# Optimization experiments

Hardware: AMD Instinct MI355X
Metric: run time of the kernel (lower is better)

## Reference

```python
import jax, jax.numpy as jnp
import numpy as np

B, N, C, H, NB = 8, 16384, 128, 512, 2  # batch, points, d_feat, mlp hidden, n_block
WIN, NH = 64, 4


def _bn(x, g, b, eps=1e-5):
    # BatchNorm1d in training mode: normalize per channel over (B, N)
    m = x.mean(axis=(0, 1))
    v = x.var(axis=(0, 1))
    return (x - m) * jax.lax.rsqrt(v + eps) * g + b


def _perm_batch(key, b, n):
    return jax.vmap(lambda k: jax.random.permutation(k, n))(jax.random.split(key, b)).astype(jnp.int32)


def setup_inputs():
    key = jax.random.key(0)
    ks = jax.random.split(key, 12)
    s = 0.02
    x = jax.random.normal(ks[0], (B, N, C), jnp.float32)
    z = jax.random.normal(ks[1], (B, N, 3), jnp.float32)
    idx_pa_1 = _perm_batch(ks[2], B, N)  # random permutation per batch row
    idx_pa_2 = _perm_batch(ks[3], B, N)
    qkv_w = jax.random.normal(ks[4], (NB, C, 3 * C), jnp.float32) * s
    proj_w = jax.random.normal(ks[5], (NB, C, C), jnp.float32) * s
    fc1_w = jax.random.normal(ks[6], (NB, C, H), jnp.float32) * s
    fc2_w = jax.random.normal(ks[7], (NB, H, C), jnp.float32) * s
    n1_g = jnp.ones((NB, C), jnp.float32)
    n1_b = jnp.zeros((NB, C), jnp.float32)
    n2_g = jnp.ones((NB, C), jnp.float32)
    n2_b = jnp.zeros((NB, C), jnp.float32)
    return {"x": x, "z": z, "idx_pa_1": idx_pa_1, "idx_pa_2": idx_pa_2,
            "qkv_w": qkv_w, "proj_w": proj_w, "fc1_w": fc1_w, "fc2_w": fc2_w,
            "n1_g": n1_g, "n1_b": n1_b, "n2_g": n2_g, "n2_b": n2_b}


def reference(x, z, idx_pa_1, idx_pa_2, qkv_w, proj_w, fc1_w, fc2_w, n1_g, n1_b, n2_g, n2_b):
    b, n, c = x.shape
    nh, dh, w = NH, c // NH, WIN
    nw = n // w
    scale = np.float32(1.0 / np.sqrt(dh))
    idx_re_1 = jnp.argsort(idx_pa_1, axis=1)  # inverse permutation
    idx_re_2 = jnp.argsort(idx_pa_2, axis=1)
    for i in range(NB):
        ip = idx_pa_1 if i % 2 == 0 else idx_pa_2
        ir = idx_re_1 if i % 2 == 0 else idx_re_2
        # SpaceExpansion: gather by random permutation
        x = jnp.take_along_axis(x, ip[:, :, None], axis=1)
        zz = jnp.take_along_axis(z, ip[:, :, None], axis=1)
        # windowed attention (pre-norm, residual)
        h = _bn(x, n1_g[i], n1_b[i])
        qkv = jnp.einsum('bnc,cd->bnd', h, qkv_w[i]).reshape(b, nw, w, 3, nh, dh)
        q, k, v = qkv[:, :, :, 0], qkv[:, :, :, 1], qkv[:, :, :, 2]
        att = jax.nn.softmax(jnp.einsum('bwqhd,bwkhd->bwhqk', q, k) * scale, axis=-1)
        o = jnp.einsum('bwhqk,bwkhd->bwqhd', att, v).reshape(b, n, c)
        x = x + jnp.einsum('bnc,cd->bnd', o, proj_w[i])
        # MLP (pre-norm, residual)
        h2 = _bn(x, n2_g[i], n2_b[i])
        x = x + jnp.einsum('bnh,hc->bnc', jax.nn.relu(jnp.einsum('bnc,ch->bnh', h2, fc1_w[i])), fc2_w[i])
        # SpaceReverse: scatter back via inverse permutation
        x = jnp.take_along_axis(x, ir[:, :, None], axis=1)
        z = jnp.take_along_axis(zz, ir[:, :, None], axis=1)
    return x, z
```

## Files before the change

### kernel.cpp

```cpp
#include <hip/hip_runtime.h>
#include <cstdint>
#include <cstddef>

typedef uint16_t u16;
typedef __bf16 bf16x8 __attribute__((ext_vector_type(8)));
typedef float f32x4 __attribute__((ext_vector_type(4)));
typedef unsigned short us4 __attribute__((ext_vector_type(4)));

#define NTOK 131072
#define CDIM 128
#define MFMA __builtin_amdgcn_mfma_f32_16x16x32_bf16

__device__ __forceinline__ u16 f2b(float f) {
    unsigned int x = __builtin_bit_cast(unsigned int, f);
    unsigned int r = (x + 0x7fffu + ((x >> 16) & 1u)) >> 16;
    return (u16)r;
}

__device__ __forceinline__ us4 pack_bn4(float4 v, const float* sc, const float* sh, int c) {
    us4 o;
    o.x = f2b(v.x * sc[c] + sh[c]);
    o.y = f2b(v.y * sc[c + 1] + sh[c + 1]);
    o.z = f2b(v.z * sc[c + 2] + sh[c + 2]);
    o.w = f2b(v.w * sc[c + 3] + sh[c + 3]);
    return o;
}

__global__ __launch_bounds__(256) void bn_init(const float* __restrict__ x,
                                               float* __restrict__ acc) {
    int tid = threadIdx.x;
    int c4 = tid & 31;
    int ro = tid >> 5;
    float4 s = {0.f, 0.f, 0.f, 0.f}, s2 = {0.f, 0.f, 0.f, 0.f};
    size_t base = ((size_t)blockIdx.x * 128 + ro) * 128 + c4 * 4;
#pragma unroll
    for (int it = 0; it < 16; ++it) {
        float4 v = *(const float4*)(x + base + (size_t)it * 1024);
        s.x += v.x; s.y += v.y; s.z += v.z; s.w += v.w;
        s2.x += v.x * v.x; s2.y += v.y * v.y; s2.z += v.z * v.z; s2.w += v.w * v.w;
    }
    __shared__ float4 a1[256], a2[256];
    a1[tid] = s; a2[tid] = s2;
    __syncthreads();
    if (tid < 128) {
        int col4 = tid >> 2, comp = tid & 3;
        float t1 = 0.f, t2 = 0.f;
#pragma unroll
        for (int r = 0; r < 8; ++r) {
            t1 += a1[r * 32 + col4][comp];
            t2 += a2[r * 32 + col4][comp];
        }
        float* st = acc + (blockIdx.x & 3) * 256;
        atomicAdd(st + tid, t1);
        atomicAdd(st + 128 + tid, t2);
    }
}

__global__ void bn_finalize(const float* __restrict__ acc, const float* __restrict__ g,
                            const float* __restrict__ b, float* __restrict__ scsh) {
    int c = threadIdx.x;
    const float invn = 1.0f / (float)NTOK;
    float s = acc[c] + acc[256 + c] + acc[512 + c] + acc[768 + c];
    float q = acc[128 + c] + acc[384 + c] + acc[640 + c] + acc[896 + c];
    float mean = s * invn;
    float var = q * invn - mean * mean;
    float sc = g[c] * rsqrtf(var + 1e-5f);
    scsh[c] = sc;
    scsh[128 + c] = b[c] - mean * sc;
}

__global__ __launch_bounds__(256) void wtrans(const float* __restrict__ w, u16* __restrict__ wt,
                                              int K, int N) {
    int t = blockIdx.x * 256 + threadIdx.x;
    if (t >= K * N) return;
    int n = t % N, k = t / N;
    wt[(size_t)n * K + k] = f2b(w[t]);
}

__global__ __launch_bounds__(256, 2) void attn_fused(
    const float* __restrict__ xsrc, float* __restrict__ xdst,
    const int* __restrict__ ip, const float* __restrict__ scsh,
    const u16* __restrict__ wq, const u16* __restrict__ wp,
    float* __restrict__ stat)
{
    __shared__ u16 hsh[64 * 128];
    __shared__ u16 qkp[4][5120];
    __shared__ u16 vt[4][32 * 72];
    __shared__ float sc[128], sh[128];
    __shared__ int ipl[64];

    int tid = threadIdx.x;
    int lane = tid & 63, wv = tid >> 6;
    int l15 = lane & 15, hi = lane >> 4;
    int b = blockIdx.x >> 8;

    if (tid < 128) { sc[tid] = scsh[tid]; sh[tid] = scsh[128 + tid]; }
    if (tid < 64) ipl[tid] = ip[blockIdx.x * 64 + tid];
    __syncthreads();

    int c4 = tid & 31;
#pragma unroll
    for (int p = 0; p < 8; ++p) {
        int row = p * 8 + (tid >> 5);
        int grow = (b << 14) + ipl[row];
        float4 v = *(const float4*)(xsrc + (size_t)grow * 128 + c4 * 4);
        us4 o = pack_bn4(v, sc, sh, c4 * 4);
        int byte = (c4 * 8) ^ ((row & 7) << 4);
        *(us4*)((char*)hsh + row * 256 + byte) = o;
    }
    __syncthreads();

    int nrow[6];
#pragma unroll
    for (int nt = 0; nt < 6; ++nt) nrow[nt] = (nt >> 1) * 128 + wv * 32 + (nt & 1) * 16;
    f32x4 acc[4][6];
#pragma unroll
    for (int q = 0; q < 4; ++q)
#pragma unroll
        for (int nt = 0; nt < 6; ++nt) acc[q][nt] = (f32x4){0.f, 0.f, 0.f, 0.f};
#pragma unroll
    for (int ks = 0; ks < 4; ++ks) {
        bf16x8 af[4];
#pragma unroll
        for (int q = 0; q < 4; ++q) {
            int row = q * 16 + l15;
            int byte = (ks * 64 + hi * 16) ^ ((row & 7) << 4);
            af[q] = *(const bf16x8*)((const char*)hsh + row * 256 + byte);
        }
#pragma unroll
        for (int nt = 0; nt < 6; ++nt) {
            bf16x8 bf = *(const bf16x8*)(wq + (size_t)(nrow[nt] + l15) * 128 + ks * 32 + hi * 8);
#pragma unroll
            for (int q = 0; q < 4; ++q)
                acc[q][nt] = MFMA(af[q], bf, acc[q][nt], 0, 0, 0);
        }
    }

    u16* qh = &qkp[wv][0];
    u16* kh = qh + 2560;
    u16* vh = &vt[wv][0];
#pragma unroll
    for (int nt = 0; nt < 6; ++nt)
#pragma unroll
        for (int q = 0; q < 4; ++q)
#pragma unroll
            for (int r = 0; r < 4; ++r) {
                int tok = q * 16 + hi * 4 + r;
                int d = (nt & 1) * 16 + l15;
                u16 val = f2b(acc[q][nt][r]);
                if (nt < 2) qh[tok * 40 + d] = val;
                else if (nt < 4) kh[tok * 40 + d] = val;
                else vh[d * 72 + tok] = val;
            }

    bf16x8 qa[4], kb[4];
#pragma unroll
    for (int t = 0; t < 4; ++t) {
        qa[t] = *(const bf16x8*)(qh + (t * 16 + l15) * 40 + hi * 8);
        kb[t] = *(const bf16x8*)(kh + (t * 16 + l15) * 40 + hi * 8);
    }
    f32x4 s[4][4];
#pragma unroll
    for (int i = 0; i < 4; ++i)
#pragma unroll
        for (int j = 0; j < 4; ++j) s[i][j] = (f32x4){0.f, 0.f, 0.f, 0.f};
#pragma unroll
    for (int qi = 0; qi < 4; ++qi)
#pragma unroll
        for (int ki = 0; ki < 4; ++ki)
            s[qi][ki] = MFMA(qa[qi], kb[ki], s[qi][ki], 0, 0, 0);

    const float scale = 0.17677669529663687f;
    float inv[4][4];
    u16* P = &qkp[wv][0];
#pragma unroll
    for (int qi = 0; qi < 4; ++qi) {
#pragma unroll
        for (int r = 0; r < 4; ++r) {
            float v0 = s[qi][0][r] * scale, v1 = s[qi][1][r] * scale;
            float v2 = s[qi][2][r] * scale, v3 = s[qi][3][r] * scale;
            float m = fmaxf(fmaxf(v0, v1), fmaxf(v2, v3));
            m = fmaxf(m, __shfl_xor(m, 1)); m = fmaxf(m, __shfl_xor(m, 2));
            m = fmaxf(m, __shfl_xor(m, 4)); m = fmaxf(m, __shfl_xor(m, 8));
            float p0 = __expf(v0 - m), p1 = __expf(v1 - m);
            float p2 = __expf(v2 - m), p3 = __expf(v3 - m);
            float sum = p0 + p1 + p2 + p3;
            sum += __shfl_xor(sum, 1); sum += __shfl_xor(sum, 2);
            sum += __shfl_xor(sum, 4); sum += __shfl_xor(sum, 8);
            inv[qi][r] = 1.0f / sum;
            int row = qi * 16 + hi * 4 + r;
            P[row * 72 + l15] = f2b(p0);
            P[row * 72 + 16 + l15] = f2b(p1);
            P[row * 72 + 32 + l15] = f2b(p2);
            P[row * 72 + 48 + l15] = f2b(p3);
        }
    }

    f32x4 o[4][2];
#pragma unroll
    for (int i = 0; i < 4; ++i)
#pragma unroll
        for (int j = 0; j < 2; ++j) o[i][j] = (f32x4){0.f, 0.f, 0.f, 0.f};
#pragma unroll
    for (int ks = 0; ks < 2; ++ks) {
        bf16x8 pa[4], vb[2];
#pragma unroll
        for (int qi = 0; qi < 4; ++qi)
            pa[qi] = *(const bf16x8*)(P + (qi * 16 + l15) * 72 + ks * 32 + hi * 8);
#pragma unroll
        for (int nt = 0; nt < 2; ++nt)
            vb[nt] = *(const bf16x8*)(vh + (nt * 16 + l15) * 72 + ks * 32 + hi * 8);
#pragma unroll
        for (int qi = 0; qi < 4; ++qi)
#pragma unroll
            for (int nt = 0; nt < 2; ++nt)
                o[qi][nt] = MFMA(pa[qi], vb[nt], o[qi][nt], 0, 0, 0);
    }

    __syncthreads();
#pragma unroll
    for (int qi = 0; qi < 4; ++qi)
#pragma unroll
        for (int nt = 0; nt < 2; ++nt)
#pragma unroll
            for (int r = 0; r < 4; ++r) {
                int tok = qi * 16 + hi * 4 + r;
                int col = wv * 32 + nt * 16 + l15;
                int byte = (col * 2) ^ ((tok & 7) << 4);
                *(u16*)((char*)hsh + tok * 256 + byte) = f2b(o[qi][nt][r] * inv[qi][r]);
            }
    __syncthreads();

    f32x4 pacc[4][2];
#pragma unroll
    for (int i = 0; i < 4; ++i)
#pragma unroll
        for (int j = 0; j < 2; ++j) pacc[i][j] = (f32x4){0.f, 0.f, 0.f, 0.f};
#pragma unroll
    for (int ks = 0; ks < 4; ++ks) {
        bf16x8 af[4];
#pragma unroll
        for (int q = 0; q < 4; ++q) {
            int row = q * 16 + l15;
            int byte = (ks * 64 + hi * 16) ^ ((row & 7) << 4);
            af[q] = *(const bf16x8*)((const char*)hsh + row * 256 + byte);
        }
#pragma unroll
        for (int nt = 0; nt < 2; ++nt) {
            bf16x8 bf = *(const bf16x8*)(wp + (size_t)(wv * 32 + nt * 16 + l15) * 128 + ks * 32 + hi * 8);
#pragma unroll
            for (int q = 0; q < 4; ++q)
                pacc[q][nt] = MFMA(af[q], bf, pacc[q][nt], 0, 0, 0);
        }
    }
    float cs[2] = {0.f, 0.f}, cq[2] = {0.f, 0.f};
#pragma unroll
    for (int qi = 0; qi < 4; ++qi)
#pragma unroll
        for (int r = 0; r < 4; ++r) {
            int tok = qi * 16 + hi * 4 + r;
            size_t grow = (size_t)((b << 14) + ipl[tok]) * 128;
#pragma unroll
            for (int nt = 0; nt < 2; ++nt) {
                int col = wv * 32 + nt * 16 + l15;
                float v = pacc[qi][nt][r] + xsrc[grow + col];
                xdst[grow + col] = v;
                cs[nt] += v; cq[nt] += v * v;
            }
        }
#pragma unroll
    for (int nt = 0; nt < 2; ++nt) {
        cs[nt] += __shfl_xor(cs[nt], 16); cs[nt] += __shfl_xor(cs[nt], 32);
        cq[nt] += __shfl_xor(cq[nt], 16); cq[nt] += __shfl_xor(cq[nt], 32);
    }
    if (lane < 16) {
        float* st = stat + (blockIdx.x & 3) * 256;
#pragma unroll
        for (int nt = 0; nt < 2; ++nt) {
            int col = wv * 32 + nt * 16 + l15;
            atomicAdd(st + col, cs[nt]);
            atomicAdd(st + 128 + col, cq[nt]);
        }
    }
}

__global__ __launch_bounds__(256, 2) void mlp_fused(
    const float* __restrict__ xsrc, float* __restrict__ xdst,
    const float* __restrict__ scsh,
    const u16* __restrict__ w1, const u16* __restrict__ w2,
    float* __restrict__ stat)
{
    __shared__ u16 hb[128 * 128];
    __shared__ u16 hc[128 * 128];
    __shared__ float sc[128], sh[128];
    int tid = threadIdx.x, lane = tid & 63, wv = tid >> 6;
    int l15 = lane & 15, hi = lane >> 4;
    int m0 = blockIdx.x * 128;
    if (tid < 128) { sc[tid] = scsh[tid]; sh[tid] = scsh[128 + tid]; }
    __syncthreads();

    int c4 = tid & 31;
#pragma unroll
    for (int p = 0; p < 16; ++p) {
        int row = p * 8 + (tid >> 5);
        float4 v = *(const float4*)(xsrc + (size_t)(m0 + row) * 128 + c4 * 4);
        us4 o = pack_bn4(v, sc, sh, c4 * 4);
        int byte = (c4 * 8) ^ ((row & 7) << 4);
        *(us4*)((char*)hb + row * 256 + byte) = o;
    }
    __syncthreads();

    int wr = (wv >> 1) * 64, wc = (wv & 1) * 64;
    f32x4 acc2[4][4];
#pragma unroll
    for (int i = 0; i < 4; ++i)
#pragma unroll
        for (int j = 0; j < 4; ++j) acc2[i][j] = (f32x4){0.f, 0.f, 0.f, 0.f};

    for (int c = 0; c < 4; ++c) {
        f32x4 acc1[4][4];
#pragma unroll
        for (int i = 0; i < 4; ++i)
#pragma unroll
            for (int j = 0; j < 4; ++j) acc1[i][j] = (f32x4){0.f, 0.f, 0.f, 0.f};
#pragma unroll
        for (int ks = 0; ks < 4; ++ks) {
            bf16x8 af[4];
#pragma unroll
            for (int q = 0; q < 4; ++q) {
                int row = wr + q * 16 + l15;
                int byte = (ks * 64 + hi * 16) ^ ((row & 7) << 4);
                af[q] = *(const bf16x8*)((const char*)hb + row * 256 + byte);
            }
#pragma unroll
            for (int nt = 0; nt < 4; ++nt) {
                bf16x8 bf = *(const bf16x8*)(w1 + (size_t)(c * 128 + wc + nt * 16 + l15) * 128 + ks * 32 + hi * 8);
#pragma unroll
                for (int q = 0; q < 4; ++q)
                    acc1[q][nt] = MFMA(af[q], bf, acc1[q][nt], 0, 0, 0);
            }
        }
        __syncthreads();
#pragma unroll
        for (int q = 0; q < 4; ++q)
#pragma unroll
            for (int nt = 0; nt < 4; ++nt)
#pragma unroll
                for (int r = 0; r < 4; ++r) {
                    int row = wr + q * 16 + hi * 4 + r;
                    int col = wc + nt * 16 + l15;
                    int byte = (col * 2) ^ ((row & 7) << 4);
                    *(u16*)((char*)hc + row * 256 + byte) = f2b(fmaxf(acc1[q][nt][r], 0.f));
                }
        __syncthreads();
#pragma unroll
        for (int ks = 0; ks < 4; ++ks) {
            bf16x8 af[4];
#pragma unroll
            for (int q = 0; q < 4; ++q) {
                int row = wr + q * 16 + l15;
                int byte = (ks * 64 + hi * 16) ^ ((row & 7) << 4);
                af[q] = *(const bf16x8*)((const char*)hc + row * 256 + byte);
            }
#pragma unroll
            for (int nt = 0; nt < 4; ++nt) {
                bf16x8 bf = *(const bf16x8*)(w2 + (size_t)(wc + nt * 16 + l15) * 512 + c * 128 + ks * 32 + hi * 8);
#pragma unroll
                for (int q = 0; q < 4; ++q)
                    acc2[q][nt] = MFMA(af[q], bf, acc2[q][nt], 0, 0, 0);
            }
        }
    }

    float cs[4] = {0.f, 0.f, 0.f, 0.f}, cq[4] = {0.f, 0.f, 0.f, 0.f};
#pragma unroll
    for (int q = 0; q < 4; ++q)
#pragma unroll
        for (int r = 0; r < 4; ++r) {
            size_t row = (size_t)(m0 + wr + q * 16 + hi * 4 + r) * 128;
#pragma unroll
            for (int nt = 0; nt < 4; ++nt) {
                int col = wc + nt * 16 + l15;
                float v = acc2[q][nt][r] + xsrc[row + col];
                xdst[row + col] = v;
                cs[nt] += v; cq[nt] += v * v;
            }
        }
    if (stat) {
#pragma unroll
        for (int nt = 0; nt < 4; ++nt) {
            cs[nt] += __shfl_xor(cs[nt], 16); cs[nt] += __shfl_xor(cs[nt], 32);
            cq[nt] += __shfl_xor(cq[nt], 16); cq[nt] += __shfl_xor(cq[nt], 32);
        }
        if (lane < 16) {
            float* st = stat + (blockIdx.x & 3) * 256;
#pragma unroll
            for (int nt = 0; nt < 4; ++nt) {
                int col = wc + nt * 16 + l15;
                atomicAdd(st + col, cs[nt]);
                atomicAdd(st + 128 + col, cq[nt]);
            }
        }
    }
}

extern "C" void kernel_launch(void* const* d_in, const int* in_sizes, int n_in,
                              void* d_out, int out_size, void* d_ws, size_t ws_size,
                              hipStream_t stream) {
    const float* x_in = (const float*)d_in[0];
    const float* z_in = (const float*)d_in[1];
    const int* ip1 = (const int*)d_in[2];
    const int* ip2 = (const int*)d_in[3];
    const float* qkv_w = (const float*)d_in[4];
    const float* proj_w = (const float*)d_in[5];
    const float* fc1_w = (const float*)d_in[6];
    const float* fc2_w = (const float*)d_in[7];
    const float* n1g = (const float*)d_in[8];
    const float* n1b = (const float*)d_in[9];
    const float* n2g = (const float*)d_in[10];
    const float* n2b = (const float*)d_in[11];

    char* ws = (char*)d_ws;
    float* xbuf = (float*)(ws + 0);
    u16* wtb = (u16*)(ws + 67108864);
    float* stats = (float*)(ws + 67895296);
    float* scsh = stats + 4096;

    float* out_x = (float*)d_out;
    float* out_z = out_x + (size_t)NTOK * CDIM;

    hipMemsetAsync(stats, 0, 4096 * sizeof(float), stream);
    hipMemcpyAsync(out_z, z_in, (size_t)NTOK * 3 * sizeof(float),
                   hipMemcpyDeviceToDevice, stream);

    for (int i = 0; i < 2; ++i) {
        wtrans<<<(128 * 384 + 255) / 256, 256, 0, stream>>>(qkv_w + (size_t)i * 128 * 384,
                                                            wtb + i * 49152, 128, 384);
        wtrans<<<(128 * 128 + 255) / 256, 256, 0, stream>>>(proj_w + (size_t)i * 128 * 128,
                                                            wtb + 98304 + i * 16384, 128, 128);
        wtrans<<<(128 * 512 + 255) / 256, 256, 0, stream>>>(fc1_w + (size_t)i * 128 * 512,
                                                            wtb + 131072 + i * 65536, 128, 512);
        wtrans<<<(512 * 128 + 255) / 256, 256, 0, stream>>>(fc2_w + (size_t)i * 512 * 128,
                                                            wtb + 262144 + i * 65536, 512, 128);
    }

    bn_init<<<1024, 256, 0, stream>>>(x_in, stats + 0);

    for (int i = 0; i < 2; ++i) {
        const int* ip = (i == 0) ? ip1 : ip2;
        const float* asrc = (i == 0) ? x_in : xbuf;
        float* S_bn1 = stats + (i == 0 ? 0 : 2048);
        float* S_bn2 = stats + (i == 0 ? 1024 : 3072);
        const u16* wt_qkv = wtb + i * 49152;
        const u16* wt_proj = wtb + 98304 + i * 16384;
        const u16* wt_fc1 = wtb + 131072 + i * 65536;
        const u16* wt_fc2 = wtb + 262144 + i * 65536;

        bn_finalize<<<1, 128, 0, stream>>>(S_bn1, n1g + i * 128, n1b + i * 128, scsh);
        attn_fused<<<2048, 256, 0, stream>>>(asrc, xbuf, ip, scsh, wt_qkv, wt_proj, S_bn2);
        bn_finalize<<<1, 128, 0, stream>>>(S_bn2, n2g + i * 128, n2b + i * 128, scsh);
        mlp_fused<<<1024, 256, 0, stream>>>(xbuf, (i == 0) ? xbuf : out_x, scsh,
                                            wt_fc1, wt_fc2,
                                            (i == 0) ? (stats + 2048) : nullptr);
    }
}
```

Measured before the change: 499.1 us.

## Rewrite attention and MLP kernels to keep QKV and scores in registers

The attention kernel now computes Q^T, K^T and V with swapped operand roles, so the QK^T and PV products run directly from registers through 16x16x16 bf16 MFMA. This removes the LDS round-trips for Q, K, V and P and shrinks shared memory to a single buffer. The MLP kernel is restructured so each wave owns 16 tokens, loads and normalizes its inputs straight into registers, and keeps the hidden tile in a per-wave LDS slice; block size drops to 64 tokens with occupancy hint 4. BN stat atomics are spread over 8 slots instead of 4. The trade-off is more weight reloads from global or L2 per token in the MLP, plus higher register pressure.

```diff
diff --git a/kernel.cpp b/kernel.cpp
--- a/kernel.cpp
+++ b/kernel.cpp
@@ -4,6 +4,8 @@
 
 typedef uint16_t u16;
 typedef __bf16 bf16x8 __attribute__((ext_vector_type(8)));
+typedef __bf16 bf16x4 __attribute__((ext_vector_type(4)));
+typedef short s16x4 __attribute__((ext_vector_type(4)));
 typedef float f32x4 __attribute__((ext_vector_type(4)));
 typedef unsigned short us4 __attribute__((ext_vector_type(4)));
 
@@ -26,6 +28,23 @@
     return o;
 }
 
+__device__ __forceinline__ s16x4 cvt4(f32x4 v) {
+    bf16x4 b;
+    b[0] = (__bf16)v[0]; b[1] = (__bf16)v[1];
+    b[2] = (__bf16)v[2]; b[3] = (__bf16)v[3];
+    return __builtin_bit_cast(s16x4, b);
+}
+
+__device__ __forceinline__ f32x4 mfma16(s16x4 a, s16x4 b, f32x4 c) {
+#if __has_builtin(__builtin_amdgcn_mfma_f32_16x16x16bf16_1k)
+    return __builtin_amdgcn_mfma_f32_16x16x16bf16_1k(a, b, c, 0, 0, 0);
+#else
+    asm volatile("s_nop 3\n\tv_mfma_f32_16x16x16_bf16 %0, %1, %2, %0\n\ts_nop 7"
+                 : "+v"(c) : "v"(a), "v"(b));
+    return c;
+#endif
+}
+
 __global__ __launch_bounds__(256) void bn_init(const float* __restrict__ x,
                                                float* __restrict__ acc) {
     int tid = threadIdx.x;
@@ -50,7 +69,7 @@
             t1 += a1[r * 32 + col4][comp];
             t2 += a2[r * 32 + col4][comp];
         }
-        float* st = acc + (blockIdx.x & 3) * 256;
+        float* st = acc + (blockIdx.x & 7) * 256;
         atomicAdd(st + tid, t1);
         atomicAdd(st + 128 + tid, t2);
     }
@@ -60,8 +79,12 @@
                             const float* __restrict__ b, float* __restrict__ scsh) {
     int c = threadIdx.x;
     const float invn = 1.0f / (float)NTOK;
-    float s = acc[c] + acc[256 + c] + acc[512 + c] + acc[768 + c];
-    float q = acc[128 + c] + acc[384 + c] + acc[640 + c] + acc[896 + c];
+    float s = 0.f, q = 0.f;
+#pragma unroll
+    for (int k = 0; k < 8; ++k) {
+        s += acc[k * 256 + c];
+        q += acc[k * 256 + 128 + c];
+    }
     float mean = s * invn;
     float var = q * invn - mean * mean;
     float sc = g[c] * rsqrtf(var + 1e-5f);
@@ -80,12 +103,10 @@
 __global__ __launch_bounds__(256, 2) void attn_fused(
     const float* __restrict__ xsrc, float* __restrict__ xdst,
     const int* __restrict__ ip, const float* __restrict__ scsh,
-    const u16* __restrict__ wq, const u16* __restrict__ wp,
+    const u16* __restrict__ wqt, const u16* __restrict__ wpt,
     float* __restrict__ stat)
 {
-    __shared__ u16 hsh[64 * 128];
-    __shared__ u16 qkp[4][5120];
-    __shared__ u16 vt[4][32 * 72];
+    __shared__ u16 buf[64 * 136];
     __shared__ float sc[128], sh[128];
     __shared__ int ipl[64];
 
@@ -105,165 +126,162 @@
         int grow = (b << 14) + ipl[row];
         float4 v = *(const float4*)(xsrc + (size_t)grow * 128 + c4 * 4);
         us4 o = pack_bn4(v, sc, sh, c4 * 4);
-        int byte = (c4 * 8) ^ ((row & 7) << 4);
-        *(us4*)((char*)hsh + row * 256 + byte) = o;
-    }
-    __syncthreads();
-
-    int nrow[6];
-#pragma unroll
-    for (int nt = 0; nt < 6; ++nt) nrow[nt] = (nt >> 1) * 128 + wv * 32 + (nt & 1) * 16;
-    f32x4 acc[4][6];
-#pragma unroll
-    for (int q = 0; q < 4; ++q)
-#pragma unroll
-        for (int nt = 0; nt < 6; ++nt) acc[q][nt] = (f32x4){0.f, 0.f, 0.f, 0.f};
+        *(us4*)(buf + row * 136 + c4 * 4) = o;
+    }
+    __syncthreads();
+
+    f32x4 aQ[2][4], aK[2][4], aV[4][2];
+#pragma unroll
+    for (int i = 0; i < 2; ++i)
+#pragma unroll
+        for (int j = 0; j < 4; ++j) { aQ[i][j] = (f32x4){0,0,0,0}; aK[i][j] = (f32x4){0,0,0,0}; }
+#pragma unroll
+    for (int i = 0; i < 4; ++i)
+#pragma unroll
+        for (int j = 0; j < 2; ++j) aV[i][j] = (f32x4){0,0,0,0};
+
+#pragma unroll
+    for (int ks = 0; ks < 4; ++ks) {
+        bf16x8 hf[4];
+#pragma unroll
+        for (int t = 0; t < 4; ++t)
+            hf[t] = *(const bf16x8*)(buf + (t * 16 + l15) * 136 + ks * 32 + hi * 8);
+        bf16x8 qf[2], kf[2], vf[2];
+#pragma unroll
+        for (int md = 0; md < 2; ++md) {
+            int rq = wv * 32 + md * 16 + l15;
+            qf[md] = *(const bf16x8*)(wqt + (size_t)rq * 128 + ks * 32 + hi * 8);
+            kf[md] = *(const bf16x8*)(wqt + (size_t)(128 + rq) * 128 + ks * 32 + hi * 8);
+            vf[md] = *(const bf16x8*)(wqt + (size_t)(256 + rq) * 128 + ks * 32 + hi * 8);
+        }
+#pragma unroll
+        for (int md = 0; md < 2; ++md)
+#pragma unroll
+            for (int nt = 0; nt < 4; ++nt) {
+                aQ[md][nt] = MFMA(qf[md], hf[nt], aQ[md][nt], 0, 0, 0);
+                aK[md][nt] = MFMA(kf[md], hf[nt], aK[md][nt], 0, 0, 0);
+            }
+#pragma unroll
+        for (int mt = 0; mt < 4; ++mt)
+#pragma unroll
+            for (int nd = 0; nd < 2; ++nd)
+                aV[mt][nd] = MFMA(hf[mt], vf[nd], aV[mt][nd], 0, 0, 0);
+    }
+
+    const float SCALE = 0.17677669529663687f;
+    s16x4 qc[2][4], kc[2][4], vc[4][2];
+#pragma unroll
+    for (int md = 0; md < 2; ++md)
+#pragma unroll
+        for (int nt = 0; nt < 4; ++nt) {
+            qc[md][nt] = cvt4(aQ[md][nt] * SCALE);
+            kc[md][nt] = cvt4(aK[md][nt]);
+        }
+#pragma unroll
+    for (int mt = 0; mt < 4; ++mt)
+#pragma unroll
+        for (int nd = 0; nd < 2; ++nd)
+            vc[mt][nd] = cvt4(aV[mt][nd]);
+
+    f32x4 s[4][4];
+#pragma unroll
+    for (int i = 0; i < 4; ++i)
+#pragma unroll
+        for (int j = 0; j < 4; ++j) s[i][j] = (f32x4){0,0,0,0};
+#pragma unroll
+    for (int kt = 0; kt < 2; ++kt)
+#pragma unroll
+        for (int mt = 0; mt < 4; ++mt)
+#pragma unroll
+            for (int nt = 0; nt < 4; ++nt)
+                s[mt][nt] = mfma16(kc[kt][mt], qc[kt][nt], s[mt][nt]);
+
+    float inv[4];
+#pragma unroll
+    for (int nt = 0; nt < 4; ++nt) {
+        float m = -1e30f;
+#pragma unroll
+        for (int mt = 0; mt < 4; ++mt)
+#pragma unroll
+            for (int r = 0; r < 4; ++r) m = fmaxf(m, s[mt][nt][r]);
+        m = fmaxf(m, __shfl_xor(m, 16));
+        m = fmaxf(m, __shfl_xor(m, 32));
+        float sum = 0.f;
+#pragma unroll
+        for (int mt = 0; mt < 4; ++mt) {
+            f32x4 e;
+#pragma unroll
+            for (int r = 0; r < 4; ++r) e[r] = __expf(s[mt][nt][r] - m);
+            sum += e[0] + e[1] + e[2] + e[3];
+            s[mt][nt] = e;
+        }
+        sum += __shfl_xor(sum, 16);
+        sum += __shfl_xor(sum, 32);
+        inv[nt] = 1.0f / sum;
+    }
+    s16x4 pc[4][4];
+#pragma unroll
+    for (int mt = 0; mt < 4; ++mt)
+#pragma unroll
+        for (int nt = 0; nt < 4; ++nt) pc[mt][nt] = cvt4(s[mt][nt]);
+
+    f32x4 o[2][4];
+#pragma unroll
+    for (int i = 0; i < 2; ++i)
+#pragma unroll
+        for (int j = 0; j < 4; ++j) o[i][j] = (f32x4){0,0,0,0};
+#pragma unroll
+    for (int kt = 0; kt < 4; ++kt)
+#pragma unroll
+        for (int md = 0; md < 2; ++md)
+#pragma unroll
+            for (int nt = 0; nt < 4; ++nt)
+                o[md][nt] = mfma16(vc[kt][md], pc[kt][nt], o[md][nt]);
+#pragma unroll
+    for (int md = 0; md < 2; ++md)
+#pragma unroll
+        for (int nt = 0; nt < 4; ++nt) o[md][nt] *= inv[nt];
+
+    __syncthreads();
+#pragma unroll
+    for (int md = 0; md < 2; ++md)
+#pragma unroll
+        for (int nt = 0; nt < 4; ++nt) {
+            s16x4 w = cvt4(o[md][nt]);
+            *(s16x4*)(buf + (nt * 16 + l15) * 136 + wv * 32 + md * 16 + hi * 4) = w;
+        }
+    __syncthreads();
+
+    f32x4 p[4][2];
+#pragma unroll
+    for (int i = 0; i < 4; ++i)
+#pragma unroll
+        for (int j = 0; j < 2; ++j) p[i][j] = (f32x4){0,0,0,0};
 #pragma unroll
     for (int ks = 0; ks < 4; ++ks) {
         bf16x8 af[4];
 #pragma unroll
-        for (int q = 0; q < 4; ++q) {
-            int row = q * 16 + l15;
-            int byte = (ks * 64 + hi * 16) ^ ((row & 7) << 4);
-            af[q] = *(const bf16x8*)((const char*)hsh + row * 256 + byte);
-        }
-#pragma unroll
-        for (int nt = 0; nt < 6; ++nt) {
-            bf16x8 bf = *(const bf16x8*)(wq + (size_t)(nrow[nt] + l15) * 128 + ks * 32 + hi * 8);
-#pragma unroll
-            for (int q = 0; q < 4; ++q)
-                acc[q][nt] = MFMA(af[q], bf, acc[q][nt], 0, 0, 0);
-        }
-    }
-
-    u16* qh = &qkp[wv][0];
-    u16* kh = qh + 2560;
-    u16* vh = &vt[wv][0];
-#pragma unroll
-    for (int nt = 0; nt < 6; ++nt)
-#pragma unroll
-        for (int q = 0; q < 4; ++q)
-#pragma unroll
-            for (int r = 0; r < 4; ++r) {
-                int tok = q * 16 + hi * 4 + r;
-                int d = (nt & 1) * 16 + l15;
-                u16 val = f2b(acc[q][nt][r]);
-                if (nt < 2) qh[tok * 40 + d] = val;
-                else if (nt < 4) kh[tok * 40 + d] = val;
-                else vh[d * 72 + tok] = val;
-            }
-
-    bf16x8 qa[4], kb[4];
-#pragma unroll
-    for (int t = 0; t < 4; ++t) {
-        qa[t] = *(const bf16x8*)(qh + (t * 16 + l15) * 40 + hi * 8);
-        kb[t] = *(const bf16x8*)(kh + (t * 16 + l15) * 40 + hi * 8);
-    }
-    f32x4 s[4][4];
-#pragma unroll
-    for (int i = 0; i < 4; ++i)
-#pragma unroll
-        for (int j = 0; j < 4; ++j) s[i][j] = (f32x4){0.f, 0.f, 0.f, 0.f};
-#pragma unroll
-    for (int qi = 0; qi < 4; ++qi)
-#pragma unroll
-        for (int ki = 0; ki < 4; ++ki)
-            s[qi][ki] = MFMA(qa[qi], kb[ki], s[qi][ki], 0, 0, 0);
-
-    const float scale = 0.17677669529663687f;
-    float inv[4][4];
-    u16* P = &qkp[wv][0];
-#pragma unroll
-    for (int qi = 0; qi < 4; ++qi) {
+        for (int t = 0; t < 4; ++t)
+            af[t] = *(const bf16x8*)(buf + (t * 16 + l15) * 136 + ks * 32 + hi * 8);
+#pragma unroll
+        for (int nt = 0; nt < 2; ++nt) {
+            bf16x8 bf = *(const bf16x8*)(wpt + (size_t)(wv * 32 + nt * 16 + l15) * 128 + ks * 32 + hi * 8);
+#pragma unroll
+            for (int t = 0; t < 4; ++t)
+                p[t][nt] = MFMA(af[t], bf, p[t][nt], 0, 0, 0);
+        }
+    }
+    float cs[2] = {0.f, 0.f}, cq[2] = {0.f, 0.f};
+#pragma unroll
+    for (int t = 0; t < 4; ++t)
 #pragma unroll
         for (int r = 0; r < 4; ++r) {
-            float v0 = s[qi][0][r] * scale, v1 = s[qi][1][r] * scale;
-            float v2 = s[qi][2][r] * scale, v3 = s[qi][3][r] * scale;
-            float m = fmaxf(fmaxf(v0, v1), fmaxf(v2, v3));
-            m = fmaxf(m, __shfl_xor(m, 1)); m = fmaxf(m, __shfl_xor(m, 2));
-            m = fmaxf(m, __shfl_xor(m, 4)); m = fmaxf(m, __shfl_xor(m, 8));
-            float p0 = __expf(v0 - m), p1 = __expf(v1 - m);
-            float p2 = __expf(v2 - m), p3 = __expf(v3 - m);
-            float sum = p0 + p1 + p2 + p3;
-            sum += __shfl_xor(sum, 1); sum += __shfl_xor(sum, 2);
-            sum += __shfl_xor(sum, 4); sum += __shfl_xor(sum, 8);
-            inv[qi][r] = 1.0f / sum;
-            int row = qi * 16 + hi * 4 + r;
-            P[row * 72 + l15] = f2b(p0);
-            P[row * 72 + 16 + l15] = f2b(p1);
-            P[row * 72 + 32 + l15] = f2b(p2);
-            P[row * 72 + 48 + l15] = f2b(p3);
-        }
-    }
-
-    f32x4 o[4][2];
-#pragma unroll
-    for (int i = 0; i < 4; ++i)
-#pragma unroll
-        for (int j = 0; j < 2; ++j) o[i][j] = (f32x4){0.f, 0.f, 0.f, 0.f};
-#pragma unroll
-    for (int ks = 0; ks < 2; ++ks) {
-        bf16x8 pa[4], vb[2];
-#pragma unroll
-        for (int qi = 0; qi < 4; ++qi)
-            pa[qi] = *(const bf16x8*)(P + (qi * 16 + l15) * 72 + ks * 32 + hi * 8);
-#pragma unroll
-        for (int nt = 0; nt < 2; ++nt)
-            vb[nt] = *(const bf16x8*)(vh + (nt * 16 + l15) * 72 + ks * 32 + hi * 8);
-#pragma unroll
-        for (int qi = 0; qi < 4; ++qi)
-#pragma unroll
-            for (int nt = 0; nt < 2; ++nt)
-                o[qi][nt] = MFMA(pa[qi], vb[nt], o[qi][nt], 0, 0, 0);
-    }
-
-    __syncthreads();
-#pragma unroll
-    for (int qi = 0; qi < 4; ++qi)
-#pragma unroll
-        for (int nt = 0; nt < 2; ++nt)
-#pragma unroll
-            for (int r = 0; r < 4; ++r) {
-                int tok = qi * 16 + hi * 4 + r;
-                int col = wv * 32 + nt * 16 + l15;
-                int byte = (col * 2) ^ ((tok & 7) << 4);
-                *(u16*)((char*)hsh + tok * 256 + byte) = f2b(o[qi][nt][r] * inv[qi][r]);
-            }
-    __syncthreads();
-
-    f32x4 pacc[4][2];
-#pragma unroll
-    for (int i = 0; i < 4; ++i)
-#pragma unroll
-        for (int j = 0; j < 2; ++j) pacc[i][j] = (f32x4){0.f, 0.f, 0.f, 0.f};
-#pragma unroll
-    for (int ks = 0; ks < 4; ++ks) {
-        bf16x8 af[4];
-#pragma unroll
-        for (int q = 0; q < 4; ++q) {
-            int row = q * 16 + l15;
-            int byte = (ks * 64 + hi * 16) ^ ((row & 7) << 4);
-            af[q] = *(const bf16x8*)((const char*)hsh + row * 256 + byte);
-        }
-#pragma unroll
-        for (int nt = 0; nt < 2; ++nt) {
-            bf16x8 bf = *(const bf16x8*)(wp + (size_t)(wv * 32 + nt * 16 + l15) * 128 + ks * 32 + hi * 8);
-#pragma unroll
-            for (int q = 0; q < 4; ++q)
-                pacc[q][nt] = MFMA(af[q], bf, pacc[q][nt], 0, 0, 0);
-        }
-    }
-    float cs[2] = {0.f, 0.f}, cq[2] = {0.f, 0.f};
-#pragma unroll
-    for (int qi = 0; qi < 4; ++qi)
-#pragma unroll
-        for (int r = 0; r < 4; ++r) {
-            int tok = qi * 16 + hi * 4 + r;
+            int tok = t * 16 + hi * 4 + r;
             size_t grow = (size_t)((b << 14) + ipl[tok]) * 128;
 #pragma unroll
             for (int nt = 0; nt < 2; ++nt) {
                 int col = wv * 32 + nt * 16 + l15;
-                float v = pacc[qi][nt][r] + xsrc[grow + col];
+                float v = p[t][nt][r] + xsrc[grow + col];
                 xdst[grow + col] = v;
                 cs[nt] += v; cq[nt] += v * v;
             }
@@ -274,7 +292,7 @@
         cq[nt] += __shfl_xor(cq[nt], 16); cq[nt] += __shfl_xor(cq[nt], 32);
     }
     if (lane < 16) {
-        float* st = stat + (blockIdx.x & 3) * 256;
+        float* st = stat + (blockIdx.x & 7) * 256;
 #pragma unroll
         for (int nt = 0; nt < 2; ++nt) {
             int col = wv * 32 + nt * 16 + l15;
@@ -284,119 +302,97 @@
     }
 }
 
-__global__ __launch_bounds__(256, 2) void mlp_fused(
+__global__ __launch_bounds__(256, 4) void mlp_fused(
     const float* __restrict__ xsrc, float* __restrict__ xdst,
     const float* __restrict__ scsh,
-    const u16* __restrict__ w1, const u16* __restrict__ w2,
+    const u16* __restrict__ w1t, const u16* __restrict__ w2t,
     float* __restrict__ stat)
 {
-    __shared__ u16 hb[128 * 128];
-    __shared__ u16 hc[128 * 128];
+    __shared__ u16 tb[4][16 * 136];
     __shared__ float sc[128], sh[128];
     int tid = threadIdx.x, lane = tid & 63, wv = tid >> 6;
     int l15 = lane & 15, hi = lane >> 4;
-    int m0 = blockIdx.x * 128;
+    int tok0 = blockIdx.x * 64 + wv * 16;
     if (tid < 128) { sc[tid] = scsh[tid]; sh[tid] = scsh[128 + tid]; }
     __syncthreads();
 
-    int c4 = tid & 31;
-#pragma unroll
-    for (int p = 0; p < 16; ++p) {
-        int row = p * 8 + (tid >> 5);
-        float4 v = *(const float4*)(xsrc + (size_t)(m0 + row) * 128 + c4 * 4);
-        us4 o = pack_bn4(v, sc, sh, c4 * 4);
-        int byte = (c4 * 8) ^ ((row & 7) << 4);
-        *(us4*)((char*)hb + row * 256 + byte) = o;
-    }
-    __syncthreads();
-
-    int wr = (wv >> 1) * 64, wc = (wv & 1) * 64;
-    f32x4 acc2[4][4];
-#pragma unroll
-    for (int i = 0; i < 4; ++i)
-#pragma unroll
-        for (int j = 0; j < 4; ++j) acc2[i][j] = (f32x4){0.f, 0.f, 0.f, 0.f};
-
-    for (int c = 0; c < 4; ++c) {
-        f32x4 acc1[4][4];
-#pragma unroll
-        for (int i = 0; i < 4; ++i)
-#pragma unroll
-            for (int j = 0; j < 4; ++j) acc1[i][j] = (f32x4){0.f, 0.f, 0.f, 0.f};
-#pragma unroll
-        for (int ks = 0; ks < 4; ++ks) {
-            bf16x8 af[4];
-#pragma unroll
-            for (int q = 0; q < 4; ++q) {
-                int row = wr + q * 16 + l15;
-                int byte = (ks * 64 + hi * 16) ^ ((row & 7) << 4);
-                af[q] = *(const bf16x8*)((const char*)hb + row * 256 + byte);
+    bf16x8 hf[4];
+#pragma unroll
+    for (int ks = 0; ks < 4; ++ks) {
+        const float* xr = xsrc + (size_t)(tok0 + l15) * 128 + ks * 32 + hi * 8;
+        float4 a = *(const float4*)xr;
+        float4 bq = *(const float4*)(xr + 4);
+        int c0 = ks * 32 + hi * 8;
+        float4 s0 = *(const float4*)&sc[c0], s1 = *(const float4*)&sc[c0 + 4];
+        float4 h0 = *(const float4*)&sh[c0], h1 = *(const float4*)&sh[c0 + 4];
+        bf16x8 h;
+        h[0] = (__bf16)(a.x * s0.x + h0.x); h[1] = (__bf16)(a.y * s0.y + h0.y);
+        h[2] = (__bf16)(a.z * s0.z + h0.z); h[3] = (__bf16)(a.w * s0.w + h0.w);
+        h[4] = (__bf16)(bq.x * s1.x + h1.x); h[5] = (__bf16)(bq.y * s1.y + h1.y);
+        h[6] = (__bf16)(bq.z * s1.z + h1.z); h[7] = (__bf16)(bq.w * s1.w + h1.w);
+        hf[ks] = h;
+    }
+
+    u16* myb = &tb[wv][0];
+    f32x4 a2[8];
+#pragma unroll
+    for (int n = 0; n < 8; ++n) a2[n] = (f32x4){0,0,0,0};
+
+#pragma unroll
+    for (int ch = 0; ch < 4; ++ch) {
+        f32x4 a1[8];
+#pragma unroll
+        for (int t = 0; t < 8; ++t) a1[t] = (f32x4){0,0,0,0};
+#pragma unroll
+        for (int ht = 0; ht < 8; ++ht)
+#pragma unroll
+            for (int ks = 0; ks < 4; ++ks) {
+                bf16x8 wf = *(const bf16x8*)(w1t + (size_t)(ch * 128 + ht * 16 + l15) * 128 + ks * 32 + hi * 8);
+                a1[ht] = MFMA(wf, hf[ks], a1[ht], 0, 0, 0);
             }
 #pragma unroll
-            for (int nt = 0; nt < 4; ++nt) {
-                bf16x8 bf = *(const bf16x8*)(w1 + (size_t)(c * 128 + wc + nt * 16 + l15) * 128 + ks * 32 + hi * 8);
-#pragma unroll
-                for (int q = 0; q < 4; ++q)
-                    acc1[q][nt] = MFMA(af[q], bf, acc1[q][nt], 0, 0, 0);
+        for (int ht = 0; ht < 8; ++ht) {
+            f32x4 v = a1[ht];
+#pragma unroll
+            for (int r = 0; r < 4; ++r) v[r] = fmaxf(v[r], 0.f);
+            *(s16x4*)(myb + l15 * 136 + ht * 16 + hi * 4) = cvt4(v);
+        }
+#pragma unroll
+        for (int kt = 0; kt < 4; ++kt) {
+            bf16x8 af = *(const bf16x8*)(myb + l15 * 136 + kt * 32 + hi * 8);
+#pragma unroll
+            for (int nt = 0; nt < 8; ++nt) {
+                bf16x8 bf = *(const bf16x8*)(w2t + (size_t)(nt * 16 + l15) * 512 + ch * 128 + kt * 32 + hi * 8);
+                a2[nt] = MFMA(af, bf, a2[nt], 0, 0, 0);
             }
         }
-        __syncthreads();
-#pragma unroll
-        for (int q = 0; q < 4; ++q)
-#pragma unroll
-            for (int nt = 0; nt < 4; ++nt)
-#pragma unroll
-                for (int r = 0; r < 4; ++r) {
-                    int row = wr + q * 16 + hi * 4 + r;
-                    int col = wc + nt * 16 + l15;
-                    int byte = (col * 2) ^ ((row & 7) << 4);
-                    *(u16*)((char*)hc + row * 256 + byte) = f2b(fmaxf(acc1[q][nt][r], 0.f));
-                }
-        __syncthreads();
-#pragma unroll
-        for (int ks = 0; ks < 4; ++ks) {
-            bf16x8 af[4];
-#pragma unroll
-            for (int q = 0; q < 4; ++q) {
-                int row = wr + q * 16 + l15;
-                int byte = (ks * 64 + hi * 16) ^ ((row & 7) << 4);
-                af[q] = *(const bf16x8*)((const char*)hc + row * 256 + byte);
-            }
-#pragma unroll
-            for (int nt = 0; nt < 4; ++nt) {
-                bf16x8 bf = *(const bf16x8*)(w2 + (size_t)(wc + nt * 16 + l15) * 512 + c * 128 + ks * 32 + hi * 8);
-#pragma unroll
-                for (int q = 0; q < 4; ++q)
-                    acc2[q][nt] = MFMA(af[q], bf, acc2[q][nt], 0, 0, 0);
-            }
-        }
-    }
-
-    float cs[4] = {0.f, 0.f, 0.f, 0.f}, cq[4] = {0.f, 0.f, 0.f, 0.f};
-#pragma unroll
-    for (int q = 0; q < 4; ++q)
-#pragma unroll
-        for (int r = 0; r < 4; ++r) {
-            size_t row = (size_t)(m0 + wr + q * 16 + hi * 4 + r) * 128;
-#pragma unroll
-            for (int nt = 0; nt < 4; ++nt) {
-                int col = wc + nt * 16 + l15;
-                float v = acc2[q][nt][r] + xsrc[row + col];
-                xdst[row + col] = v;
-                cs[nt] += v; cq[nt] += v * v;
-            }
-        }
+    }
+
+    float cs[8], cq[8];
+#pragma unroll
+    for (int n = 0; n < 8; ++n) { cs[n] = 0.f; cq[n] = 0.f; }
+#pragma unroll
+    for (int r = 0; r < 4; ++r) {
+        size_t row = (size_t)(tok0 + hi * 4 + r) * 128;
+#pragma unroll
+        for (int nt = 0; nt < 8; ++nt) {
+            int col = nt * 16 + l15;
+            float v = a2[nt][r] + xsrc[row + col];
+            xdst[row + col] = v;
+            cs[nt] += v; cq[nt] += v * v;
+        }
+    }
     if (stat) {
 #pragma unroll
-        for (int nt = 0; nt < 4; ++nt) {
+        for (int nt = 0; nt < 8; ++nt) {
             cs[nt] += __shfl_xor(cs[nt], 16); cs[nt] += __shfl_xor(cs[nt], 32);
             cq[nt] += __shfl_xor(cq[nt], 16); cq[nt] += __shfl_xor(cq[nt], 32);
         }
         if (lane < 16) {
-            float* st = stat + (blockIdx.x & 3) * 256;
-#pragma unroll
-            for (int nt = 0; nt < 4; ++nt) {
-                int col = wc + nt * 16 + l15;
+            float* st = stat + (blockIdx.x & 7) * 256;
+#pragma unroll
+            for (int nt = 0; nt < 8; ++nt) {
+                int col = nt * 16 + l15;
                 atomicAdd(st + col, cs[nt]);
                 atomicAdd(st + 128 + col, cq[nt]);
             }
@@ -424,12 +420,12 @@
     float* xbuf = (float*)(ws + 0);
     u16* wtb = (u16*)(ws + 67108864);
     float* stats = (float*)(ws + 67895296);
-    float* scsh = stats + 4096;
+    float* scsh = stats + 4 * 2048;
 
     float* out_x = (float*)d_out;
     float* out_z = out_x + (size_t)NTOK * CDIM;
 
-    hipMemsetAsync(stats, 0, 4096 * sizeof(float), stream);
+    hipMemsetAsync(stats, 0, 4 * 2048 * sizeof(float), stream);
     hipMemcpyAsync(out_z, z_in, (size_t)NTOK * 3 * sizeof(float),
                    hipMemcpyDeviceToDevice, stream);
 
@@ -449,8 +445,8 @@
     for (int i = 0; i < 2; ++i) {
         const int* ip = (i == 0) ? ip1 : ip2;
         const float* asrc = (i == 0) ? x_in : xbuf;
-        float* S_bn1 = stats + (i == 0 ? 0 : 2048);
-        float* S_bn2 = stats + (i == 0 ? 1024 : 3072);
+        float* S_bn1 = stats + (i == 0 ? 0 : 2 * 2048);
+        float* S_bn2 = stats + (i == 0 ? 1 * 2048 : 3 * 2048);
         const u16* wt_qkv = wtb + i * 49152;
         const u16* wt_proj = wtb + 98304 + i * 16384;
         const u16* wt_fc1 = wtb + 131072 + i * 65536;
@@ -459,8 +455,8 @@
         bn_finalize<<<1, 128, 0, stream>>>(S_bn1, n1g + i * 128, n1b + i * 128, scsh);
         attn_fused<<<2048, 256, 0, stream>>>(asrc, xbuf, ip, scsh, wt_qkv, wt_proj, S_bn2);
         bn_finalize<<<1, 128, 0, stream>>>(S_bn2, n2g + i * 128, n2b + i * 128, scsh);
-        mlp_fused<<<1024, 256, 0, stream>>>(xbuf, (i == 0) ? xbuf : out_x, scsh,
+        mlp_fused<<<2048, 256, 0, stream>>>(xbuf, (i == 0) ? xbuf : out_x, scsh,
                                             wt_fc1, wt_fc2,
-                                            (i == 0) ? (stats + 2048) : nullptr);
-    }
-}
+                                            (i == 0) ? (stats + 2 * 2048) : nullptr);
+    }
+}
```

Result: slower. 788.0 us (+57.9%).
